# Performance work log

Measured on AMD Instinct MI355X. Metric: run time of the kernel, lower is better.

The kernel has to match this reference:

```python
import jax, jax.numpy as jnp
import numpy as np

B, S, D, H, E, F = 2, 1024, 1024, 16, 8, 4096
HD = D // H
EPS = 1e-5


def setup_inputs() -> dict:
    key = jax.random.key(0)
    ks = jax.random.split(key, 16)
    sc = 0.02
    return {
        "src": jax.random.normal(ks[0], (B, S, D), jnp.float32),
        "in_proj_w": jax.random.normal(ks[1], (3 * D, D), jnp.float32) * sc,
        "in_proj_b": jnp.zeros((3 * D,), jnp.float32),
        "out_w": jax.random.normal(ks[2], (D, D), jnp.float32) * sc,
        "out_b": jnp.zeros((D,), jnp.float32),
        "gate_w": jax.random.normal(ks[3], (E, D), jnp.float32) * sc,
        "gate_b": jnp.zeros((E,), jnp.float32),
        "w1": jax.random.normal(ks[4], (E, F, D), jnp.float32) * sc,
        "b1": jnp.zeros((E, F), jnp.float32),
        "w2": jax.random.normal(ks[5], (E, D, F), jnp.float32) * sc,
        "b2": jnp.zeros((E, D), jnp.float32),
        "ln1_g": jnp.ones((D,), jnp.float32),
        "ln1_b": jnp.zeros((D,), jnp.float32),
        "ln2_g": jnp.ones((D,), jnp.float32),
        "ln2_b": jnp.zeros((D,), jnp.float32),
    }


def layer_norm(x, g, b):
    mu = jnp.mean(x, axis=-1, keepdims=True)
    var = jnp.mean(jnp.square(x - mu), axis=-1, keepdims=True)
    return (x - mu) * jax.lax.rsqrt(var + EPS) * g + b


def mha(x, in_proj_w, in_proj_b, out_w, out_b):
    # torch nn.MultiheadAttention, batch_first, self-attention, eval mode
    qkv = x @ in_proj_w.T + in_proj_b  # (B,S,3D)
    q, k, v = jnp.split(qkv, 3, axis=-1)
    q = q.reshape(B, S, H, HD).transpose(0, 2, 1, 3)  # bhsd
    k = k.reshape(B, S, H, HD).transpose(0, 2, 1, 3)
    v = v.reshape(B, S, H, HD).transpose(0, 2, 1, 3)
    scores = jnp.einsum("bhqd,bhkd->bhqk", q, k) / np.sqrt(HD).astype(np.float32)
    attn = jax.nn.softmax(scores, axis=-1)
    o = jnp.einsum("bhqk,bhkd->bhqd", attn, v)
    o = o.transpose(0, 2, 1, 3).reshape(B, S, D)
    return o @ out_w.T + out_b


def moe(x, gate_w, gate_b, w1, b1, w2, b2, top_k=2):
    gate_logits = x @ gate_w.T + gate_b  # (B,S,E)
    topk_logits, topk_idx = jax.lax.top_k(gate_logits, top_k)
    topk_probs = jax.nn.softmax(topk_logits, axis=-1)  # (B,S,K)
    # dense per-expert weight: prob if in top-k else 0
    onehot = jax.nn.one_hot(topk_idx, E, dtype=x.dtype)  # (B,S,K,E)
    w_dense = jnp.einsum("bske,bsk->bse", onehot, topk_probs)
    # faithful to original: all experts computed densely, then mask-weighted
    h = jnp.einsum("bsd,efd->besf", x, w1) + b1[None, :, None, :]
    h = jax.nn.gelu(h, approximate=False)
    eo = jnp.einsum("besf,edf->besd", h, w2) + b2[None, :, None, :]
    out = jnp.einsum("besd,bse->bsd", eo, w_dense)
    usage = jnp.mean(jax.nn.softmax(gate_logits, axis=-1), axis=(0, 1))
    aux_loss = E * jnp.sum(usage ** 2)
    return out, aux_loss


def reference(src, in_proj_w, in_proj_b, out_w, out_b, gate_w, gate_b,
              w1, b1, w2, b2, ln1_g, ln1_b, ln2_g, ln2_b):
    attn_out = mha(src, in_proj_w, in_proj_b, out_w, out_b)
    x = layer_norm(src + attn_out, ln1_g, ln1_b)
    moe_out, aux_loss = moe(x, gate_w, gate_b, w1, b1, w2, b2)
    x = layer_norm(x + moe_out, ln2_g, ln2_b)
    return x, aux_loss
```

## Files before the change

### kernel.cpp

```cpp
#include <hip/hip_runtime.h>
#include <stdint.h>
#include <stddef.h>

#define T_TOK 2048
#define DMODEL 1024
#define NHEAD 16
#define HDIM 64
#define NEXP 8
#define FDIM 4096
#define SLEN 1024
#define NBATCH 2
#define LN_EPS 1e-5f

typedef unsigned short u16;
typedef __attribute__((ext_vector_type(8))) short s16x8;
typedef __attribute__((ext_vector_type(4))) float f32x4;
typedef __attribute__((ext_vector_type(4))) unsigned short u16x4;
typedef __attribute__((ext_vector_type(8))) unsigned short u16x8;

typedef __attribute__((address_space(1))) void gvoid;
typedef __attribute__((address_space(3))) void lvoid;

__device__ __forceinline__ u16 f2bf(float x) {
  union { float f; unsigned int u; } v; v.f = x;
  unsigned int r = v.u + 0x7fffu + ((v.u >> 16) & 1u);
  return (u16)(r >> 16);
}

__device__ __forceinline__ void gl_lds16(const u16* g, u16* lds_base) {
  __builtin_amdgcn_global_load_lds((gvoid*)g, (lvoid*)lds_base, 16, 0, 0);
}

__device__ __forceinline__ float gelu_fast(float v) {
  float vv = v * v;
  float e = __expf(v * (-1.5957691216f - 0.0713548162f * vv));
  return v * __builtin_amdgcn_rcpf(1.f + e);
}

__device__ __forceinline__ void cvt_body(const float* __restrict__ x,
                                         u16* __restrict__ y, long n4) {
  long i = (long)blockIdx.x * 256 + threadIdx.x;
  if (i >= n4) return;
  float4 v = ((const float4*)x)[i];
  u16x4 o;
  o[0] = f2bf(v.x); o[1] = f2bf(v.y); o[2] = f2bf(v.z); o[3] = f2bf(v.w);
  ((u16x4*)y)[i] = o;
}
__global__ __launch_bounds__(256) void cvt_small(const float* x, u16* y, long n4) { cvt_body(x, y, n4); }
__global__ __launch_bounds__(256) void cvt_w1(const float* x, u16* y, long n4) { cvt_body(x, y, n4); }
__global__ __launch_bounds__(256) void cvt_w2(const float* x, u16* y, long n4) { cvt_body(x, y, n4); }

template<int BM, int OUTBF, int DOGELU>
__device__ __forceinline__ void gemm_body(
    const u16* __restrict__ A, long lda,
    const u16* __restrict__ Bp, long ldb,
    char* __restrict__ C, long ldc,
    const float* __restrict__ bias,
    int Mloc, int k0start, int Kc, int m0, int n0) {
  constexpr int AS_BYTES = 2 * BM * 64 * 2;
  constexpr int SMEM_BYTES = AS_BYTES + 2 * 128 * 64 * 2;
  __shared__ __align__(16) char smem[SMEM_BYTES];
  u16 (*As)[BM][64]  = reinterpret_cast<u16(*)[BM][64]>(smem);
  u16 (*Bs)[128][64] = reinterpret_cast<u16(*)[128][64]>(smem + AS_BYTES);

  constexpr int SM = BM / 32;
  constexpr int NPA = BM / 32;
  constexpr int LPI = NPA + 4;

  int tid = threadIdx.x;
  int lane = tid & 63, w = tid >> 6;
  int lrow = lane >> 3;
  int sg8 = ((lane & 7) ^ lrow) * 8;
  int q = lane >> 4, rr = lane & 15;
  int wm = (w & 1) * (BM / 2), wn = (w >> 1) * 64;
  int NIT = Kc >> 6;

  const u16* aP[NPA];
  const u16* bP[4];
#pragma unroll
  for (int p = 0; p < NPA; p++) {
    int gr = m0 + p * 32 + w * 8 + lrow;
    if (gr > Mloc - 1) gr = Mloc - 1;
    aP[p] = A + (long)gr * lda + k0start + sg8;
  }
#pragma unroll
  for (int p = 0; p < 4; p++)
    bP[p] = Bp + (long)(n0 + p * 32 + w * 8 + lrow) * ldb + k0start + sg8;

  auto issue = [&](int b) {
#pragma unroll
    for (int p = 0; p < NPA; p++) {
      gl_lds16(aP[p], &As[b][p * 32 + w * 8][0]);
      aP[p] += 64;
    }
#pragma unroll
    for (int p = 0; p < 4; p++) {
      gl_lds16(bP[p], &Bs[b][p * 32 + w * 8][0]);
      bP[p] += 64;
    }
  };

  f32x4 acc[SM][4];
  for (int i = 0; i < SM; i++)
    for (int j = 0; j < 4; j++)
      for (int r = 0; r < 4; r++) acc[i][j][r] = 0.f;

  issue(0);
  if (NIT > 1) issue(1);

  int slot0 = ((q ^ (rr & 7)) * 8);
  int slot1 = (((4 + q) ^ (rr & 7)) * 8);

  for (int kt = 0; kt < NIT; kt++) {
    int b = kt & 1;
    if (kt + 1 < NIT)
      asm volatile("s_waitcnt vmcnt(%0)" :: "i"(LPI) : "memory");
    else
      asm volatile("s_waitcnt vmcnt(0)" ::: "memory");
    asm volatile("s_barrier" ::: "memory");

    s16x8 a0[SM], a1[SM], b0[4], b1[4];
    for (int i = 0; i < SM; i++) {
      a0[i] = *(const s16x8*)&As[b][wm + i * 16 + rr][slot0];
      a1[i] = *(const s16x8*)&As[b][wm + i * 16 + rr][slot1];
    }
    for (int j = 0; j < 4; j++) {
      b0[j] = *(const s16x8*)&Bs[b][wn + j * 16 + rr][slot0];
      b1[j] = *(const s16x8*)&Bs[b][wn + j * 16 + rr][slot1];
    }
    asm volatile("s_waitcnt lgkmcnt(0)" ::: "memory");
    asm volatile("s_barrier" ::: "memory");
    if (kt + 2 < NIT) issue(b);

    for (int i = 0; i < SM; i++)
      for (int j = 0; j < 4; j++) {
        acc[i][j] = __builtin_amdgcn_mfma_f32_16x16x32_bf16(a0[i], b0[j], acc[i][j], 0, 0, 0);
        acc[i][j] = __builtin_amdgcn_mfma_f32_16x16x32_bf16(a1[i], b1[j], acc[i][j], 0, 0, 0);
      }
  }

  u16*   Cu = (u16*)smem;
  float* Cf = (float*)smem;
  for (int i = 0; i < SM; i++)
    for (int j = 0; j < 4; j++) {
      int col = wn + j * 16 + rr;
      float bv = bias ? bias[n0 + col] : 0.f;
      for (int r = 0; r < 4; r++) {
        int row = wm + i * 16 + q * 4 + r;
        float v = acc[i][j][r] + bv;
        if (DOGELU) v = gelu_fast(v);
        if (OUTBF) Cu[row * 128 + col] = f2bf(v);
        else       Cf[row * 128 + col] = v;
      }
    }
  __syncthreads();
  if (OUTBF) {
    for (int p = 0; p < BM / 16; p++) {
      int row = p * 16 + (tid >> 4);
      int co  = (tid & 15) * 8;
      if (m0 + row < Mloc) {
        u16x8 vv = *(const u16x8*)&Cu[row * 128 + co];
        *(u16x8*)((u16*)C + (long)(m0 + row) * ldc + n0 + co) = vv;
      }
    }
  } else {
    for (int p = 0; p < BM / 8; p++) {
      int row = p * 8 + (tid >> 5);
      int co  = (tid & 31) * 4;
      if (m0 + row < Mloc) {
        float4 vv = *(const float4*)&Cf[row * 128 + co];
        *(float4*)((float*)C + (long)(m0 + row) * ldc + n0 + co) = vv;
      }
    }
  }
}

__global__ __launch_bounds__(256) void k_qkv(const u16* __restrict__ A,
                                             const u16* __restrict__ B,
                                             u16* __restrict__ C,
                                             const float* __restrict__ bias) {
  gemm_body<128, 1, 0>(A, DMODEL, B, DMODEL, (char*)C, 3 * DMODEL, bias,
                       T_TOK, 0, DMODEL, blockIdx.y * 128, blockIdx.x * 128);
}

__global__ __launch_bounds__(256) void k_outp(const u16* __restrict__ A,
                                              const u16* __restrict__ B,
                                              float* __restrict__ Cpart) {
  int z = blockIdx.z;
  char* C = (char*)(Cpart + (long)z * T_TOK * DMODEL);
  gemm_body<64, 0, 0>(A, DMODEL, B, DMODEL, C, DMODEL, nullptr,
                      T_TOK, z * 512, 512, blockIdx.y * 64, blockIdx.x * 128);
}

__global__ __launch_bounds__(256) void k_ffn1(const u16* __restrict__ Ag,
                                              const u16* __restrict__ Bg,
                                              u16* __restrict__ Cg,
                                              const float* __restrict__ biasg,
                                              const int* __restrict__ cntp,
                                              const int* __restrict__ offp) {
  int z = blockIdx.z;
  int Mloc = cntp[z];
  int m0 = blockIdx.y * 128;
  if (m0 >= Mloc) return;
  long o = offp[z];
  gemm_body<128, 1, 1>(Ag + o * DMODEL, DMODEL,
                       Bg + (long)z * FDIM * DMODEL, DMODEL,
                       (char*)(Cg + o * FDIM), FDIM,
                       biasg + (long)z * FDIM,
                       Mloc, 0, DMODEL, m0, blockIdx.x * 128);
}

__global__ __launch_bounds__(256) void k_ffn2(const u16* __restrict__ Ag,
                                              const u16* __restrict__ Bg,
                                              float* __restrict__ Cpart,
                                              const int* __restrict__ cntp,
                                              const int* __restrict__ offp) {
  int zz = blockIdx.z;
  int z = zz & 7, kh = zz >> 3;
  int Mloc = cntp[z];
  int m0 = blockIdx.y * 128;
  if (m0 >= Mloc) return;
  long o = offp[z];
  float* C = Cpart + (long)kh * 2 * T_TOK * DMODEL;
  gemm_body<128, 0, 0>(Ag + o * FDIM, FDIM,
                       Bg + (long)z * DMODEL * FDIM, FDIM,
                       (char*)(C + o * DMODEL), DMODEL,
                       nullptr,
                       Mloc, kh * 2048, 2048, m0, blockIdx.x * 128);
}

__global__ __launch_bounds__(256) void transpose_v(const u16* __restrict__ qkv,
                                                   u16* __restrict__ vt) {
  __shared__ u16 tile[64][65];
  int s0 = blockIdx.x * 64, bh = blockIdx.y;
  int b = bh >> 4, h = bh & 15;
  int r = threadIdx.x >> 3, c = (threadIdx.x & 7) * 8;
  for (int p = 0; p < 64; p += 32) {
    u16x8 v = *(const u16x8*)&qkv[(long)(b * SLEN + s0 + p + r) * 3072 + 2048 + h * 64 + c];
    for (int j = 0; j < 8; j++) tile[p + r][c + j] = v[j];
  }
  __syncthreads();
  for (int p = 0; p < 64; p += 32) {
    int d = p + r;
    u16x8 v;
    for (int j = 0; j < 8; j++) v[j] = tile[c + j][d];
    *(u16x8*)&vt[((long)bh * 64 + d) * SLEN + s0 + c] = v;
  }
}

__global__ __launch_bounds__(256) void fused_attn(const u16* __restrict__ qkv,
                                                  const u16* __restrict__ vt,
                                                  u16* __restrict__ o2) {
  __shared__ u16 Qs[128][64];
  __shared__ u16 Ks[2][64][64];
  __shared__ u16 Vs[2][64][64];
  __shared__ u16 Ps[128][72];

  int qt = blockIdx.x, bh = blockIdx.y;
  int b = bh >> 4, h = bh & 15;
  const u16* base = qkv + (long)b * SLEN * 3072 + h * 64;
  const u16* vbase = vt + (long)bh * HDIM * SLEN;

  int tid = threadIdx.x, lane = tid & 63, w = tid >> 6;
  int lrow = lane >> 3;
  int sg8 = ((lane & 7) ^ lrow) * 8;
  int q = lane >> 4, rr = lane & 15;
  int wm = w * 32;

  auto issue_kv = [&](int kt, int bf) {
    for (int p = 0; p < 2; p++) {
      int rb = p * 32 + w * 8;
      gl_lds16(base + (long)(kt * 64 + rb + lrow) * 3072 + 1024 + sg8, &Ks[bf][rb][0]);
      gl_lds16(vbase + (long)(rb + lrow) * SLEN + kt * 64 + sg8, &Vs[bf][rb][0]);
    }
  };

  for (int p = 0; p < 4; p++) {
    int rb = p * 32 + w * 8;
    gl_lds16(base + (long)(qt * 128 + rb + lrow) * 3072 + sg8, &Qs[rb][0]);
  }
  issue_kv(0, 0);

  f32x4 O[2][4];
  float mi[2][4], li[2][4];
  for (int i = 0; i < 2; i++)
    for (int r = 0; r < 4; r++) { mi[i][r] = -1e30f; li[i][r] = 0.f; }
  for (int i = 0; i < 2; i++)
    for (int jn = 0; jn < 4; jn++)
      for (int r = 0; r < 4; r++) O[i][jn][r] = 0.f;

  for (int kt = 0; kt < 16; kt++) {
    int bf = kt & 1;
    asm volatile("s_waitcnt vmcnt(0)" ::: "memory");
    asm volatile("s_barrier" ::: "memory");
    if (kt + 1 < 16) issue_kv(kt + 1, bf ^ 1);

    f32x4 S[2][4];
    for (int i = 0; i < 2; i++)
      for (int j = 0; j < 4; j++)
        for (int r = 0; r < 4; r++) S[i][j][r] = 0.f;
    for (int ks = 0; ks < 2; ks++) {
      int slot = (((ks * 4 + q) ^ (rr & 7)) * 8);
      s16x8 aq0 = *(const s16x8*)&Qs[wm + rr][slot];
      s16x8 aq1 = *(const s16x8*)&Qs[wm + 16 + rr][slot];
      for (int j = 0; j < 4; j++) {
        s16x8 bk = *(const s16x8*)&Ks[bf][j * 16 + rr][slot];
        S[0][j] = __builtin_amdgcn_mfma_f32_16x16x32_bf16(aq0, bk, S[0][j], 0, 0, 0);
        S[1][j] = __builtin_amdgcn_mfma_f32_16x16x32_bf16(aq1, bk, S[1][j], 0, 0, 0);
      }
    }

    for (int i = 0; i < 2; i++) {
      for (int r = 0; r < 4; r++) {
        float mx = -1e30f;
        for (int j = 0; j < 4; j++) mx = fmaxf(mx, S[i][j][r]);
        for (int o = 1; o < 16; o <<= 1) mx = fmaxf(mx, __shfl_xor(mx, o));
        mx *= 0.125f;
        float mnew = fmaxf(mi[i][r], mx);
        float al = __expf(mi[i][r] - mnew);
        mi[i][r] = mnew;
        float ps = 0.f;
        for (int j = 0; j < 4; j++) {
          float e = __expf(S[i][j][r] * 0.125f - mnew);
          S[i][j][r] = e;
          ps += e;
        }
        for (int o = 1; o < 16; o <<= 1) ps += __shfl_xor(ps, o);
        li[i][r] = li[i][r] * al + ps;
        for (int jn = 0; jn < 4; jn++) O[i][jn][r] *= al;
      }
    }

    for (int i = 0; i < 2; i++)
      for (int j = 0; j < 4; j++)
        for (int r = 0; r < 4; r++)
          Ps[wm + i * 16 + q * 4 + r][j * 16 + rr] = f2bf(S[i][j][r]);

    for (int ks = 0; ks < 2; ks++) {
      s16x8 ap0 = *(const s16x8*)&Ps[wm + rr][ks * 32 + q * 8];
      s16x8 ap1 = *(const s16x8*)&Ps[wm + 16 + rr][ks * 32 + q * 8];
      int slot = (((ks * 4 + q) ^ (rr & 7)) * 8);
      for (int jn = 0; jn < 4; jn++) {
        s16x8 bv = *(const s16x8*)&Vs[bf][jn * 16 + rr][slot];
        O[0][jn] = __builtin_amdgcn_mfma_f32_16x16x32_bf16(ap0, bv, O[0][jn], 0, 0, 0);
        O[1][jn] = __builtin_amdgcn_mfma_f32_16x16x32_bf16(ap1, bv, O[1][jn], 0, 0, 0);
      }
    }
  }

  __syncthreads();
  u16* Pf = &Ps[0][0];
  for (int i = 0; i < 2; i++)
    for (int r = 0; r < 4; r++) {
      float inv = 1.f / li[i][r];
      int row = wm + i * 16 + q * 4 + r;
      for (int jn = 0; jn < 4; jn++)
        Pf[row * 64 + jn * 16 + rr] = f2bf(O[i][jn][r] * inv);
    }
  __syncthreads();
  for (int p = 0; p < 4; p++) {
    int row = p * 32 + (tid >> 3);
    int co  = (tid & 7) * 8;
    u16x8 vv = *(const u16x8*)&Pf[row * 64 + co];
    int s = qt * 128 + row;
    *(u16x8*)&o2[((long)(b * SLEN + s)) * DMODEL + h * 64 + co] = vv;
  }
}

__global__ __launch_bounds__(256) void add_ln(const float* __restrict__ a,
                                              const float* __restrict__ p0,
                                              const float* __restrict__ p1,
                                              const float* __restrict__ ob,
                                              const float* __restrict__ g,
                                              const float* __restrict__ bb,
                                              float* __restrict__ xf, u16* __restrict__ xb) {
  int t = blockIdx.x, tid = threadIdx.x;
  float4 va = ((const float4*)(a + (long)t * DMODEL))[tid];
  float4 v0v = ((const float4*)(p0 + (long)t * DMODEL))[tid];
  float4 v1v = ((const float4*)(p1 + (long)t * DMODEL))[tid];
  float4 vo = ((const float4*)ob)[tid];
  float v0 = va.x + v0v.x + v1v.x + vo.x;
  float v1 = va.y + v0v.y + v1v.y + vo.y;
  float v2 = va.z + v0v.z + v1v.z + vo.z;
  float v3 = va.w + v0v.w + v1v.w + vo.w;
  float s = v0 + v1 + v2 + v3;
  float s2 = v0 * v0 + v1 * v1 + v2 * v2 + v3 * v3;
  __shared__ float sa[4], sb[4];
  for (int o = 32; o; o >>= 1) { s += __shfl_down(s, o); s2 += __shfl_down(s2, o); }
  int lane = tid & 63, w = tid >> 6;
  if (lane == 0) { sa[w] = s; sb[w] = s2; }
  __syncthreads();
  s = sa[0] + sa[1] + sa[2] + sa[3];
  s2 = sb[0] + sb[1] + sb[2] + sb[3];
  float mu = s * (1.f / DMODEL);
  float var = s2 * (1.f / DMODEL) - mu * mu;
  float rs = rsqrtf(var + LN_EPS);
  float4 gg = ((const float4*)g)[tid];
  float4 bv = ((const float4*)bb)[tid];
  float4 o;
  o.x = (v0 - mu) * rs * gg.x + bv.x;
  o.y = (v1 - mu) * rs * gg.y + bv.y;
  o.z = (v2 - mu) * rs * gg.z + bv.z;
  o.w = (v3 - mu) * rs * gg.w + bv.w;
  ((float4*)(xf + (long)t * DMODEL))[tid] = o;
  u16x4 obv;
  obv[0] = f2bf(o.x); obv[1] = f2bf(o.y); obv[2] = f2bf(o.z); obv[3] = f2bf(o.w);
  ((u16x4*)(xb + (long)t * DMODEL))[tid] = obv;
}

__global__ __launch_bounds__(256) void gate_kernel(
    const float* __restrict__ xf, const float* __restrict__ gw, const float* __restrict__ gb,
    int* __restrict__ cnt, int* __restrict__ tok_list,
    int* __restrict__ tk_e, int* __restrict__ tk_pos, float* __restrict__ tk_prob,
    float* __restrict__ usage) {
  int wid = threadIdx.x >> 6, lane = threadIdx.x & 63;
  int t = blockIdx.x * 4 + wid;
  float xv[16];
  for (int j = 0; j < 16; j++) xv[j] = xf[(long)t * DMODEL + j * 64 + lane];
  float l[8];
  for (int e = 0; e < 8; e++) {
    float d = 0.f;
    for (int j = 0; j < 16; j++) d += xv[j] * gw[e * DMODEL + j * 64 + lane];
    for (int o = 32; o; o >>= 1) d += __shfl_down(d, o);
    l[e] = d;
  }
  __shared__ float us[8];
  if (threadIdx.x < 8) us[threadIdx.x] = 0.f;
  __syncthreads();
  if (lane == 0) {
    float mx = -1e30f;
    for (int e = 0; e < 8; e++) { l[e] += gb[e]; mx = fmaxf(mx, l[e]); }
    float ex[8], sum = 0.f;
    for (int e = 0; e < 8; e++) { ex[e] = expf(l[e] - mx); sum += ex[e]; }
    float inv = 1.f / sum;
    for (int e = 0; e < 8; e++) atomicAdd(&us[e], ex[e] * inv);
    int i1 = 0;
    for (int e = 1; e < 8; e++) if (l[e] > l[i1]) i1 = e;
    int i2 = (i1 == 0) ? 1 : 0;
    for (int e = 0; e < 8; e++) if (e != i1 && l[e] > l[i2]) i2 = e;
    float bb = expf(l[i2] - l[i1]);
    float p1 = 1.f / (1.f + bb), p2 = bb / (1.f + bb);
    int pos1 = atomicAdd(&cnt[i1], 1);
    tok_list[i1 * 2048 + pos1] = t;
    tk_e[2 * t] = i1; tk_pos[2 * t] = pos1; tk_prob[2 * t] = p1;
    int pos2 = atomicAdd(&cnt[i2], 1);
    tok_list[i2 * 2048 + pos2] = t;
    tk_e[2 * t + 1] = i2; tk_pos[2 * t + 1] = pos2; tk_prob[2 * t + 1] = p2;
  }
  __syncthreads();
  if (threadIdx.x < 8) atomicAdd(&usage[threadIdx.x], us[threadIdx.x]);
}

__global__ void finalize_gate(const int* __restrict__ cnt, int* __restrict__ offp,
                              const float* __restrict__ usage, float* __restrict__ aux_out) {
  if (threadIdx.x == 0) {
    int o = 0;
    for (int e = 0; e < 8; e++) { offp[e] = o; o += cnt[e]; }
    float s = 0.f;
    for (int e = 0; e < 8; e++) { float u = usage[e] * (1.f / T_TOK); s += u * u; }
    aux_out[0] = (float)NEXP * s;
  }
}

__global__ __launch_bounds__(256) void gather_x(const u16* __restrict__ xb,
                                                const int* __restrict__ cnt,
                                                const int* __restrict__ offp,
                                                const int* __restrict__ tok_list,
                                                u16* __restrict__ xg) {
  int e = blockIdx.y, i = blockIdx.x;
  if (i >= cnt[e]) return;
  int t = tok_list[e * 2048 + i];
  long j = offp[e] + i;
  ((uint2*)(xg + j * DMODEL))[threadIdx.x] =
      ((const uint2*)(xb + (long)t * DMODEL))[threadIdx.x];
}

__global__ __launch_bounds__(256) void moe_ln2(
    const float* __restrict__ xf, const float* __restrict__ y,
    const float* __restrict__ b2g,
    const int* __restrict__ offp, const int* __restrict__ tk_e,
    const int* __restrict__ tk_pos, const float* __restrict__ tk_prob,
    const float* __restrict__ g, const float* __restrict__ bb, float* __restrict__ out) {
  const long HALF = (long)2 * T_TOK * DMODEL;
  int t = blockIdx.x, tid = threadIdx.x;
  int e0 = tk_e[2 * t], e1 = tk_e[2 * t + 1];
  long j0 = (long)offp[e0] + tk_pos[2 * t];
  long j1 = (long)offp[e1] + tk_pos[2 * t + 1];
  float p0 = tk_prob[2 * t], p1 = tk_prob[2 * t + 1];
  float4 vx = ((const float4*)(xf + (long)t * DMODEL))[tid];
  float4 y0a = ((const float4*)(y + j0 * DMODEL))[tid];
  float4 y0b = ((const float4*)(y + HALF + j0 * DMODEL))[tid];
  float4 y1a = ((const float4*)(y + j1 * DMODEL))[tid];
  float4 y1b = ((const float4*)(y + HALF + j1 * DMODEL))[tid];
  float4 b0v = ((const float4*)(b2g + (long)e0 * DMODEL))[tid];
  float4 b1v = ((const float4*)(b2g + (long)e1 * DMODEL))[tid];
  float v0 = vx.x + p0 * (y0a.x + y0b.x + b0v.x) + p1 * (y1a.x + y1b.x + b1v.x);
  float v1 = vx.y + p0 * (y0a.y + y0b.y + b0v.y) + p1 * (y1a.y + y1b.y + b1v.y);
  float v2 = vx.z + p0 * (y0a.z + y0b.z + b0v.z) + p1 * (y1a.z + y1b.z + b1v.z);
  float v3 = vx.w + p0 * (y0a.w + y0b.w + b0v.w) + p1 * (y1a.w + y1b.w + b1v.w);
  float s = v0 + v1 + v2 + v3;
  float s2 = v0 * v0 + v1 * v1 + v2 * v2 + v3 * v3;
  __shared__ float sa[4], sb[4];
  for (int o = 32; o; o >>= 1) { s += __shfl_down(s, o); s2 += __shfl_down(s2, o); }
  int lane = tid & 63, w = tid >> 6;
  if (lane == 0) { sa[w] = s; sb[w] = s2; }
  __syncthreads();
  s = sa[0] + sa[1] + sa[2] + sa[3];
  s2 = sb[0] + sb[1] + sb[2] + sb[3];
  float mu = s * (1.f / DMODEL);
  float var = s2 * (1.f / DMODEL) - mu * mu;
  float rs = rsqrtf(var + LN_EPS);
  float4 gg = ((const float4*)g)[tid];
  float4 bv = ((const float4*)bb)[tid];
  float4 o;
  o.x = (v0 - mu) * rs * gg.x + bv.x;
  o.y = (v1 - mu) * rs * gg.y + bv.y;
  o.z = (v2 - mu) * rs * gg.z + bv.z;
  o.w = (v3 - mu) * rs * gg.w + bv.w;
  ((float4*)(out + (long)t * DMODEL))[tid] = o;
}

extern "C" void kernel_launch(void* const* d_in, const int* in_sizes, int n_in,
                              void* d_out, int out_size, void* d_ws, size_t ws_size,
                              hipStream_t stream) {
  const float* src  = (const float*)d_in[0];
  const float* inw  = (const float*)d_in[1];
  const float* inb  = (const float*)d_in[2];
  const float* outw = (const float*)d_in[3];
  const float* outb = (const float*)d_in[4];
  const float* gw   = (const float*)d_in[5];
  const float* gb   = (const float*)d_in[6];
  const float* w1   = (const float*)d_in[7];
  const float* b1   = (const float*)d_in[8];
  const float* w2   = (const float*)d_in[9];
  const float* b2   = (const float*)d_in[10];
  const float* g1   = (const float*)d_in[11];
  const float* bb1  = (const float*)d_in[12];
  const float* g2   = (const float*)d_in[13];
  const float* bb2  = (const float*)d_in[14];
  float* out = (float*)d_out;

  char* w = (char*)d_ws;
  auto alloc = [&](size_t bytes) {
    char* p = w;
    w += (bytes + 255) & ~(size_t)255;
    return p;
  };

  int*   cnt     = (int*)alloc(8 * 4);
  int*   offp    = (int*)alloc(8 * 4);
  float* usage   = (float*)alloc(8 * 4);
  int*   tok_list= (int*)alloc((size_t)NEXP * 2048 * 4);
  int*   tk_e    = (int*)alloc((size_t)2 * T_TOK * 4);
  int*   tk_pos  = (int*)alloc((size_t)2 * T_TOK * 4);
  float* tk_prob = (float*)alloc((size_t)2 * T_TOK * 4);

  u16* src_bf  = (u16*)alloc((size_t)T_TOK * DMODEL * 2);
  u16* inw_bf  = (u16*)alloc((size_t)3 * DMODEL * DMODEL * 2);
  u16* outw_bf = (u16*)alloc((size_t)DMODEL * DMODEL * 2);
  u16* w1_bf   = (u16*)alloc((size_t)NEXP * FDIM * DMODEL * 2);
  u16* w2_bf   = (u16*)alloc((size_t)NEXP * DMODEL * FDIM * 2);
  u16* qkv_bf  = (u16*)alloc((size_t)T_TOK * 3 * DMODEL * 2);
  u16* vt_bf   = (u16*)alloc((size_t)T_TOK * DMODEL * 2);
  u16* o2_bf   = (u16*)alloc((size_t)T_TOK * DMODEL * 2);
  float* attn_p= (float*)alloc((size_t)2 * T_TOK * DMODEL * 4);
  float* x_f   = (float*)alloc((size_t)T_TOK * DMODEL * 4);
  u16* x_bf    = (u16*)alloc((size_t)T_TOK * DMODEL * 2);
  u16* xg_bf   = (u16*)alloc((size_t)2 * T_TOK * DMODEL * 2);
  u16* h_bf    = (u16*)alloc((size_t)2 * T_TOK * FDIM * 2);
  float* y_f   = (float*)alloc((size_t)4 * T_TOK * DMODEL * 4);
  (void)ws_size; (void)n_in; (void)in_sizes; (void)out_size;

  hipMemsetAsync(cnt, 0, 3 * 256, stream);

  cvt_small<<<(T_TOK * DMODEL / 4 + 255) / 256, 256, 0, stream>>>(src, src_bf, T_TOK * DMODEL / 4);
  cvt_small<<<(3 * DMODEL * DMODEL / 4 + 255) / 256, 256, 0, stream>>>(inw, inw_bf, 3L * DMODEL * DMODEL / 4);
  cvt_small<<<(DMODEL * DMODEL / 4 + 255) / 256, 256, 0, stream>>>(outw, outw_bf, (long)DMODEL * DMODEL / 4);
  cvt_w1<<<(int)((long)NEXP * FDIM * DMODEL / 4 / 256), 256, 0, stream>>>(w1, w1_bf, (long)NEXP * FDIM * DMODEL / 4);
  cvt_w2<<<(int)((long)NEXP * DMODEL * FDIM / 4 / 256), 256, 0, stream>>>(w2, w2_bf, (long)NEXP * DMODEL * FDIM / 4);

  k_qkv<<<dim3(24, 16), 256, 0, stream>>>(src_bf, inw_bf, qkv_bf, inb);

  transpose_v<<<dim3(16, 32), 256, 0, stream>>>(qkv_bf, vt_bf);

  fused_attn<<<dim3(8, 32), 256, 0, stream>>>(qkv_bf, vt_bf, o2_bf);

  k_outp<<<dim3(8, 32, 2), 256, 0, stream>>>(o2_bf, outw_bf, attn_p);

  add_ln<<<T_TOK, 256, 0, stream>>>(src, attn_p, attn_p + (long)T_TOK * DMODEL,
                                    outb, g1, bb1, x_f, x_bf);

  gate_kernel<<<T_TOK / 4, 256, 0, stream>>>(x_f, gw, gb, cnt, tok_list,
                                             tk_e, tk_pos, tk_prob, usage);
  finalize_gate<<<1, 64, 0, stream>>>(cnt, offp, usage, out + (long)T_TOK * DMODEL);

  gather_x<<<dim3(2048, 8), 256, 0, stream>>>(x_bf, cnt, offp, tok_list, xg_bf);

  k_ffn1<<<dim3(32, 16, 8), 256, 0, stream>>>(xg_bf, w1_bf, h_bf, b1, cnt, offp);

  k_ffn2<<<dim3(8, 16, 16), 256, 0, stream>>>(h_bf, w2_bf, y_f, cnt, offp);

  moe_ln2<<<T_TOK, 256, 0, stream>>>(x_f, y_f, b2, offp, tk_e, tk_pos, tk_prob,
                                     g2, bb2, out);
}
```

Before: 634.0 us.

## Overlap expert weight conversion with attention kernels and fuse token gather into FFN1

The separate w1 and w2 fp32-to-bf16 conversion kernels are removed. Their work now runs on extra blocks appended to the QKV GEMM and fused attention launches, using grid-stride loops, so the bandwidth-bound conversion can overlap with compute-bound attention work. The gather_x kernel and its staging buffer are also removed: FFN1 now reads rows of x_bf indirectly through the token list when it builds its A-tile pointers. This saves one launch and one round trip through memory, but the extra conversion blocks may compete for CUs and delay the GEMM and attention tiles.

```diff
diff --git a/kernel.cpp b/kernel.cpp
--- a/kernel.cpp
+++ b/kernel.cpp
@@ -37,8 +37,19 @@
   return v * __builtin_amdgcn_rcpf(1.f + e);
 }
 
-__device__ __forceinline__ void cvt_body(const float* __restrict__ x,
-                                         u16* __restrict__ y, long n4) {
+__device__ __forceinline__ void cvt_stride(const float* __restrict__ x,
+                                           u16* __restrict__ y,
+                                           long n4, long i0, long stride) {
+  for (long i = i0; i < n4; i += stride) {
+    float4 v = ((const float4*)x)[i];
+    u16x4 o;
+    o[0] = f2bf(v.x); o[1] = f2bf(v.y); o[2] = f2bf(v.z); o[3] = f2bf(v.w);
+    ((u16x4*)y)[i] = o;
+  }
+}
+
+__global__ __launch_bounds__(256) void cvt_small(const float* __restrict__ x,
+                                                 u16* __restrict__ y, long n4) {
   long i = (long)blockIdx.x * 256 + threadIdx.x;
   if (i >= n4) return;
   float4 v = ((const float4*)x)[i];
@@ -46,9 +57,6 @@
   o[0] = f2bf(v.x); o[1] = f2bf(v.y); o[2] = f2bf(v.z); o[3] = f2bf(v.w);
   ((u16x4*)y)[i] = o;
 }
-__global__ __launch_bounds__(256) void cvt_small(const float* x, u16* y, long n4) { cvt_body(x, y, n4); }
-__global__ __launch_bounds__(256) void cvt_w1(const float* x, u16* y, long n4) { cvt_body(x, y, n4); }
-__global__ __launch_bounds__(256) void cvt_w2(const float* x, u16* y, long n4) { cvt_body(x, y, n4); }
 
 template<int BM, int OUTBF, int DOGELU>
 __device__ __forceinline__ void gemm_body(
@@ -56,7 +64,8 @@
     const u16* __restrict__ Bp, long ldb,
     char* __restrict__ C, long ldc,
     const float* __restrict__ bias,
-    int Mloc, int k0start, int Kc, int m0, int n0) {
+    int Mloc, int k0start, int Kc, int m0, int n0,
+    const int* __restrict__ gather = nullptr) {
   constexpr int AS_BYTES = 2 * BM * 64 * 2;
   constexpr int SMEM_BYTES = AS_BYTES + 2 * 128 * 64 * 2;
   __shared__ __align__(16) char smem[SMEM_BYTES];
@@ -81,7 +90,8 @@
   for (int p = 0; p < NPA; p++) {
     int gr = m0 + p * 32 + w * 8 + lrow;
     if (gr > Mloc - 1) gr = Mloc - 1;
-    aP[p] = A + (long)gr * lda + k0start + sg8;
+    long arow = gather ? (long)gather[gr] : (long)gr;
+    aP[p] = A + arow * lda + k0start + sg8;
   }
 #pragma unroll
   for (int p = 0; p < 4; p++)
@@ -178,9 +188,19 @@
 __global__ __launch_bounds__(256) void k_qkv(const u16* __restrict__ A,
                                              const u16* __restrict__ B,
                                              u16* __restrict__ C,
-                                             const float* __restrict__ bias) {
+                                             const float* __restrict__ bias,
+                                             const float* __restrict__ w1src,
+                                             u16* __restrict__ w1dst) {
+  int id = blockIdx.x;
+  if (id >= 384) {
+    const long N4 = (long)NEXP * FDIM * DMODEL / 4;
+    cvt_stride(w1src, w1dst, N4,
+               (long)(id - 384) * 256 + threadIdx.x, 512L * 256);
+    return;
+  }
+  int x = id % 24, y = id / 24;
   gemm_body<128, 1, 0>(A, DMODEL, B, DMODEL, (char*)C, 3 * DMODEL, bias,
-                       T_TOK, 0, DMODEL, blockIdx.y * 128, blockIdx.x * 128);
+                       T_TOK, 0, DMODEL, y * 128, x * 128);
 }
 
 __global__ __launch_bounds__(256) void k_outp(const u16* __restrict__ A,
@@ -192,22 +212,24 @@
                       T_TOK, z * 512, 512, blockIdx.y * 64, blockIdx.x * 128);
 }
 
-__global__ __launch_bounds__(256) void k_ffn1(const u16* __restrict__ Ag,
+__global__ __launch_bounds__(256) void k_ffn1(const u16* __restrict__ xb,
                                               const u16* __restrict__ Bg,
                                               u16* __restrict__ Cg,
                                               const float* __restrict__ biasg,
                                               const int* __restrict__ cntp,
-                                              const int* __restrict__ offp) {
+                                              const int* __restrict__ offp,
+                                              const int* __restrict__ tok_list) {
   int z = blockIdx.z;
   int Mloc = cntp[z];
   int m0 = blockIdx.y * 128;
   if (m0 >= Mloc) return;
   long o = offp[z];
-  gemm_body<128, 1, 1>(Ag + o * DMODEL, DMODEL,
+  gemm_body<128, 1, 1>(xb, DMODEL,
                        Bg + (long)z * FDIM * DMODEL, DMODEL,
                        (char*)(Cg + o * FDIM), FDIM,
                        biasg + (long)z * FDIM,
-                       Mloc, 0, DMODEL, m0, blockIdx.x * 128);
+                       Mloc, 0, DMODEL, m0, blockIdx.x * 128,
+                       tok_list + z * 2048);
 }
 
 __global__ __launch_bounds__(256) void k_ffn2(const u16* __restrict__ Ag,
@@ -250,13 +272,22 @@
 
 __global__ __launch_bounds__(256) void fused_attn(const u16* __restrict__ qkv,
                                                   const u16* __restrict__ vt,
-                                                  u16* __restrict__ o2) {
+                                                  u16* __restrict__ o2,
+                                                  const float* __restrict__ w2src,
+                                                  u16* __restrict__ w2dst) {
   __shared__ u16 Qs[128][64];
   __shared__ u16 Ks[2][64][64];
   __shared__ u16 Vs[2][64][64];
   __shared__ u16 Ps[128][72];
 
-  int qt = blockIdx.x, bh = blockIdx.y;
+  int id = blockIdx.x;
+  if (id >= 256) {
+    const long N4 = (long)NEXP * DMODEL * FDIM / 4;
+    cvt_stride(w2src, w2dst, N4,
+               (long)(id - 256) * 256 + threadIdx.x, 512L * 256);
+    return;
+  }
+  int qt = id & 7, bh = id >> 3;
   int b = bh >> 4, h = bh & 15;
   const u16* base = qkv + (long)b * SLEN * 3072 + h * 64;
   const u16* vbase = vt + (long)bh * HDIM * SLEN;
@@ -460,19 +491,6 @@
     for (int e = 0; e < 8; e++) { float u = usage[e] * (1.f / T_TOK); s += u * u; }
     aux_out[0] = (float)NEXP * s;
   }
-}
-
-__global__ __launch_bounds__(256) void gather_x(const u16* __restrict__ xb,
-                                                const int* __restrict__ cnt,
-                                                const int* __restrict__ offp,
-                                                const int* __restrict__ tok_list,
-                                                u16* __restrict__ xg) {
-  int e = blockIdx.y, i = blockIdx.x;
-  if (i >= cnt[e]) return;
-  int t = tok_list[e * 2048 + i];
-  long j = offp[e] + i;
-  ((uint2*)(xg + j * DMODEL))[threadIdx.x] =
-      ((const uint2*)(xb + (long)t * DMODEL))[threadIdx.x];
 }
 
 __global__ __launch_bounds__(256) void moe_ln2(
@@ -566,7 +584,6 @@
   float* attn_p= (float*)alloc((size_t)2 * T_TOK * DMODEL * 4);
   float* x_f   = (float*)alloc((size_t)T_TOK * DMODEL * 4);
   u16* x_bf    = (u16*)alloc((size_t)T_TOK * DMODEL * 2);
-  u16* xg_bf   = (u16*)alloc((size_t)2 * T_TOK * DMODEL * 2);
   u16* h_bf    = (u16*)alloc((size_t)2 * T_TOK * FDIM * 2);
   float* y_f   = (float*)alloc((size_t)4 * T_TOK * DMODEL * 4);
   (void)ws_size; (void)n_in; (void)in_sizes; (void)out_size;
@@ -576,14 +593,12 @@
   cvt_small<<<(T_TOK * DMODEL / 4 + 255) / 256, 256, 0, stream>>>(src, src_bf, T_TOK * DMODEL / 4);
   cvt_small<<<(3 * DMODEL * DMODEL / 4 + 255) / 256, 256, 0, stream>>>(inw, inw_bf, 3L * DMODEL * DMODEL / 4);
   cvt_small<<<(DMODEL * DMODEL / 4 + 255) / 256, 256, 0, stream>>>(outw, outw_bf, (long)DMODEL * DMODEL / 4);
-  cvt_w1<<<(int)((long)NEXP * FDIM * DMODEL / 4 / 256), 256, 0, stream>>>(w1, w1_bf, (long)NEXP * FDIM * DMODEL / 4);
-  cvt_w2<<<(int)((long)NEXP * DMODEL * FDIM / 4 / 256), 256, 0, stream>>>(w2, w2_bf, (long)NEXP * DMODEL * FDIM / 4);
-
-  k_qkv<<<dim3(24, 16), 256, 0, stream>>>(src_bf, inw_bf, qkv_bf, inb);
+
+  k_qkv<<<896, 256, 0, stream>>>(src_bf, inw_bf, qkv_bf, inb, w1, w1_bf);
 
   transpose_v<<<dim3(16, 32), 256, 0, stream>>>(qkv_bf, vt_bf);
 
-  fused_attn<<<dim3(8, 32), 256, 0, stream>>>(qkv_bf, vt_bf, o2_bf);
+  fused_attn<<<768, 256, 0, stream>>>(qkv_bf, vt_bf, o2_bf, w2, w2_bf);
 
   k_outp<<<dim3(8, 32, 2), 256, 0, stream>>>(o2_bf, outw_bf, attn_p);
 
@@ -594,9 +609,7 @@
                                              tk_e, tk_pos, tk_prob, usage);
   finalize_gate<<<1, 64, 0, stream>>>(cnt, offp, usage, out + (long)T_TOK * DMODEL);
 
-  gather_x<<<dim3(2048, 8), 256, 0, stream>>>(x_bf, cnt, offp, tok_list, xg_bf);
-
-  k_ffn1<<<dim3(32, 16, 8), 256, 0, stream>>>(xg_bf, w1_bf, h_bf, b1, cnt, offp);
+  k_ffn1<<<dim3(32, 16, 8), 256, 0, stream>>>(x_bf, w1_bf, h_bf, b1, cnt, offp, tok_list);
 
   k_ffn2<<<dim3(8, 16, 16), 256, 0, stream>>>(h_bf, w2_bf, y_f, cnt, offp);
 
```

After: 639.7 us. No clear change (+0.9%).
